# Performance work log

Hardware: AMD Instinct MI355X
Metric: run time of the kernel (lower is better)

Reference implementation:

```python
import jax, jax.numpy as jnp
import numpy as np

B, T, DM, DS = 8, 2048, 1024, 256
BASE_DECAY = 0.05


def _lin(k, out_dim, in_dim):
    return jax.random.normal(k, (out_dim, in_dim), jnp.float32) / np.sqrt(in_dim).astype(np.float32)


def setup_inputs() -> dict:
    key = jax.random.key(0)
    ks = jax.random.split(key, 18)
    return {
        "x": jax.random.normal(ks[0], (B, T, DM), jnp.float32),
        "prev_state": jax.random.normal(ks[1], (B, DS), jnp.float32),
        "W_in": _lin(ks[2], DS, DM),
        "W_x": _lin(ks[3], DS, DM),
        "W_s": _lin(ks[4], DS, DS),
        "W_out": _lin(ks[5], DM, DS),
        "W_gx": _lin(ks[6], DS, DM),
        "b_gx": jax.random.normal(ks[7], (DS,), jnp.float32) * 0.02,
        "W_gs": _lin(ks[8], DS, DS),
        "b_gs": jax.random.normal(ks[9], (DS,), jnp.float32) * 0.02,
        "W_dc": _lin(ks[10], DS, DM + DS),
        "b_dc": jax.random.normal(ks[11], (DS,), jnp.float32) * 0.02,
        "W_pp": _lin(ks[12], DS, 2 * DS),
        "b_pp": jax.random.normal(ks[13], (DS,), jnp.float32) * 0.02,
        "W_pg": _lin(ks[14], DS, DS),
        "b_pg": jax.random.normal(ks[15], (DS,), jnp.float32) * 0.02,
    }


def reference(x, prev_state, W_in, W_x, W_s, W_out, W_gx, b_gx, W_gs, b_gs,
              W_dc, b_dc, W_pp, b_pp, W_pg, b_pg):
    # torch Linear: y = x @ W.T (+ b); W is [out, in]
    lin = lambda v, W: jnp.einsum('bti,oi->bto', v, W)
    Bx, Tx, _ = x.shape
    delta = lin(x, W_in)                                   # [B,T,DS]
    s_prev = jnp.broadcast_to(prev_state[:, None, :], (Bx, Tx, prev_state.shape[-1]))
    ctx = jnp.concatenate([x, s_prev], axis=-1)            # [B,T,DM+DS]
    decay = jnp.exp(-BASE_DECAY * jnp.clip(jax.nn.sigmoid(lin(ctx, W_dc) + b_dc), 0.0, 1.0))
    s_pred = s_prev * decay + delta + lin(x, W_x) + 0.5 * lin(s_prev, W_s)
    perturb_in = jnp.concatenate([s_pred, s_prev], axis=-1)  # [B,T,2*DS]
    perturb_vec = jnp.tanh(lin(perturb_in, W_pp) + b_pp)
    perturb_strength = jax.nn.sigmoid(lin(s_prev, W_pg) + b_pg)
    s_corrected = s_pred + perturb_strength * perturb_vec
    gate_in = jax.nn.sigmoid(lin(x, W_gx) + b_gx)
    gate_state = jax.nn.sigmoid(lin(s_prev, W_gs) + b_gs)
    h = s_corrected * gate_in * gate_state
    out = lin(h, W_out)                                    # [B,T,DM]
    return out, h[:, -1, :]
```

## Files before the change

kernel.cpp:

```cpp
#include <hip/hip_runtime.h>
#include <hip/hip_bf16.h>
#include <math.h>


typedef __attribute__((ext_vector_type(4)))  float f32x4;
typedef __attribute__((ext_vector_type(8)))  short bf16x8;

#define DEV static __device__ __forceinline__

DEV float bf2f(short u) {
  union { float f; unsigned i; } v; v.i = ((unsigned)(unsigned short)u) << 16; return v.f;
}
DEV short f2bf(float f) {
  union { float f; unsigned i; } v; v.f = f;
  unsigned x = v.i;
  return (short)((x + 0x7fffu + ((x >> 16) & 1u)) >> 16);
}
DEV unsigned pk_bf16(float lo, float hi) {
  __hip_bfloat162 h = __float22bfloat162_rn(make_float2(lo, hi));
  return *(unsigned*)&h;
}
DEV float sigmoidf_(float x) { return 1.f / (1.f + expf(-x)); }

DEV void gl16(const void* g, void* l) {
  __builtin_amdgcn_global_load_lds(
      (const __attribute__((address_space(1))) void*)(g),
      (__attribute__((address_space(3))) void*)(l), 16, 0, 0);
}

DEV void stage_tile(const short* gA, const short* gB, short* As, short* Bs,
                    int lda, int ldb, int w, int lane) {
  const int rsub = lane >> 2, kc = (lane & 3) * 8;
#pragma unroll
  for (int j = 0; j < 2; ++j) {
    const int seg = w * 2 + j;
    const int r = seg * 16 + rsub;
    gl16(gA + (size_t)r * lda + kc, As + seg * 512);
    gl16(gB + (size_t)r * ldb + kc, Bs + seg * 512);
  }
}

DEV void kstep(const short* Asb, const short* Bsb, int wr, int wc, int arow, int ag,
               f32x4 (&acc)[4][4]) {
  bf16x8 af[4], bfv[4];
#pragma unroll
  for (int mi = 0; mi < 4; ++mi)
    af[mi] = *(const bf16x8*)(Asb + (wr * 64 + mi * 16 + arow) * 32 + ag * 8);
#pragma unroll
  for (int ni = 0; ni < 4; ++ni)
    bfv[ni] = *(const bf16x8*)(Bsb + (wc * 64 + ni * 16 + arow) * 32 + ag * 8);
#pragma unroll
  for (int mi = 0; mi < 4; ++mi)
#pragma unroll
    for (int ni = 0; ni < 4; ++ni)
      acc[mi][ni] = __builtin_amdgcn_mfma_f32_16x16x32_bf16(af[mi], bfv[ni], acc[mi][ni], 0, 0, 0);
}

static const size_t OFF_S    = 0;
static const size_t OFF_G    = 8388608;
static const size_t OFF_XBF  = 25165824;
static const size_t OFF_WCAT = OFF_XBF + 33554432;
static const size_t OFF_WPP  = OFF_WCAT + 1572864;
static const size_t OFF_WOUT = OFF_WPP + 131072;
static const size_t OFF_VEC  = OFF_WOUT + 524288;

__global__ __launch_bounds__(256, 1) void prep_all_k(
    const float* __restrict__ x, short* __restrict__ xbf,
    const float* __restrict__ W_in, const float* __restrict__ W_x,
    const float* __restrict__ W_gx, const float* __restrict__ W_dc,
    const float* __restrict__ W_pp, const float* __restrict__ W_out,
    short* __restrict__ wcat, short* __restrict__ wpp, short* __restrict__ wout,
    const float* __restrict__ prev, const float* __restrict__ Ws,
    const float* __restrict__ bdc, const float* __restrict__ bpp,
    const float* __restrict__ Wpg, const float* __restrict__ bpg,
    const float* __restrict__ Wgs, const float* __restrict__ bgs,
    float* __restrict__ vecs) {
  const int bid = (int)blockIdx.x, tid = (int)threadIdx.x;
  if (bid < 8192) {
    const size_t i = ((size_t)bid * 256 + tid) * 8;
    const float4 a = *(const float4*)(x + i);
    const float4 b = *(const float4*)(x + i + 4);
    uint4 o;
    o.x = pk_bf16(a.x, a.y); o.y = pk_bf16(a.z, a.w);
    o.z = pk_bf16(b.x, b.y); o.w = pk_bf16(b.z, b.w);
    *(uint4*)(xbf + i) = o;
  } else if (bid < 12544) {
    const int idx = (bid - 8192) * 256 + tid;
    const int N_WCAT = 768 * 1024, N_WPP = 256 * 256;
    if (idx < N_WCAT) {
      const int r = idx >> 10, k = idx & 1023;
      const int g = r / 96, j = r % 96;
      float v;
      if (j < 32)      v = W_in[(g * 32 + j) * 1024 + k] + W_x[(g * 32 + j) * 1024 + k];
      else if (j < 64) v = W_gx[(g * 32 + j - 32) * 1024 + k];
      else             v = W_dc[(g * 32 + j - 64) * 1280 + k];
      wcat[idx] = f2bf(v);
    } else if (idx < N_WCAT + N_WPP) {
      const int j = idx - N_WCAT, o = j >> 8, k = j & 255;
      wpp[j] = f2bf(W_pp[o * 512 + k]);
    } else {
      const int j = idx - N_WCAT - N_WPP, o = j >> 8, k = j & 255;
      wout[j] = f2bf(W_out[o * 256 + k]);
    }
  } else {
    const int sb = bid - 12544;
    const int b = sb / 20, rem = sb % 20, m = rem >> 2, oq = rem & 3;
    const int lane = tid & 63, w = tid >> 6;
    const float4 sv = *(const float4*)(prev + b * 256 + lane * 4);
    const float* Wb; const float* bias; int stride, off;
    if (m == 0)      { Wb = W_dc; stride = 1280; off = 1024; bias = bdc; }
    else if (m == 1) { Wb = Ws;   stride = 256;  off = 0;    bias = nullptr; }
    else if (m == 2) { Wb = W_pp; stride = 512;  off = 256;  bias = bpp; }
    else if (m == 3) { Wb = Wpg;  stride = 256;  off = 0;    bias = bpg; }
    else             { Wb = Wgs;  stride = 256;  off = 0;    bias = bgs; }
    const int o0 = oq * 64 + w * 16;
#pragma unroll 4
    for (int i = 0; i < 16; ++i) {
      const int o = o0 + i;
      const float4 wv = *(const float4*)(Wb + (size_t)o * stride + off + lane * 4);
      float p = wv.x * sv.x + wv.y * sv.y + wv.z * sv.z + wv.w * sv.w;
#pragma unroll
      for (int d = 32; d >= 1; d >>= 1) p += __shfl_xor(p, d, 64);
      if (lane == 0) {
        float r = (m == 1) ? 0.5f * p : p + bias[o];
        if (m >= 3) r = sigmoidf_(r);
        vecs[m * 2048 + b * 256 + o] = r;
      }
    }
  }
}

__global__ __launch_bounds__(256) void gemm1sg_k(const short* __restrict__ A,
                                                 const short* __restrict__ Bm,
                                                 const float* __restrict__ prev,
                                                 const float* __restrict__ bgx,
                                                 const float* __restrict__ vecs,
                                                 short* __restrict__ S,
                                                 short* __restrict__ G) {
  __shared__ short As[2][4096];
  __shared__ short Bs[2][3072];
  const int tid = (int)threadIdx.x, lane = tid & 63, w = tid >> 6;
  int bid = (int)blockIdx.x;
  bid = (bid & 7) * 128 + (bid >> 3);
  const int mt = bid >> 3, ntg = bid & 7;
  const int m0 = mt * 128, b = m0 >> 11;
  const short* gA = A + (size_t)m0 * 1024;
  const short* gB = Bm + (size_t)(ntg * 96) * 1024;
  const int rsub = lane >> 2, kc = (lane & 3) * 8;

  f32x4 acc[2][6];
#pragma unroll
  for (int mi = 0; mi < 2; ++mi)
#pragma unroll
    for (int ni = 0; ni < 6; ++ni)
#pragma unroll
      for (int r = 0; r < 4; ++r) acc[mi][ni][r] = 0.f;

#define STAGE1(buf, t)                                                        \
  {                                                                           \
    _Pragma("unroll")                                                         \
    for (int j = 0; j < 2; ++j) {                                             \
      const int seg = w * 2 + j;                                              \
      gl16(gA + (size_t)(seg * 16 + rsub) * 1024 + (t) * 32 + kc,             \
           As[buf] + seg * 512);                                              \
    }                                                                         \
    {                                                                         \
      const int Gr = w * 64 + lane;                                           \
      gl16(gB + (size_t)(Gr >> 2) * 1024 + (t) * 32 + ((Gr & 3) * 8),         \
           Bs[buf] + w * 512);                                                \
    }                                                                         \
    if (w < 2) {                                                              \
      const int Gr = 256 + w * 64 + lane;                                     \
      gl16(gB + (size_t)(Gr >> 2) * 1024 + (t) * 32 + ((Gr & 3) * 8),         \
           Bs[buf] + 2048 + w * 512);                                         \
    }                                                                         \
  }

  STAGE1(0, 0);
  __syncthreads();
  const int arow = lane & 15, ag = lane >> 4;
#pragma unroll 1
  for (int t = 0; t < 32; ++t) {
    if (t < 31) STAGE1((t + 1) & 1, t + 1);
    const short* Asb = As[t & 1];
    const short* Bsb = Bs[t & 1];
    bf16x8 af[2];
#pragma unroll
    for (int mi = 0; mi < 2; ++mi)
      af[mi] = *(const bf16x8*)(Asb + (w * 32 + mi * 16 + arow) * 32 + ag * 8);
#pragma unroll
    for (int ni = 0; ni < 6; ++ni) {
      const bf16x8 bf = *(const bf16x8*)(Bsb + (ni * 16 + arow) * 32 + ag * 8);
#pragma unroll
      for (int mi = 0; mi < 2; ++mi)
        acc[mi][ni] = __builtin_amdgcn_mfma_f32_16x16x32_bf16(af[mi], bf, acc[mi][ni], 0, 0, 0);
    }
    __syncthreads();
  }
#undef STAGE1

  const int quad = lane >> 4;
#pragma unroll
  for (int nj = 0; nj < 2; ++nj) {
    const int cg = ntg * 32 + nj * 16 + arow;
    const float sdc = vecs[0 * 2048 + b * 256 + cg];
    const float sws = vecs[1 * 2048 + b * 256 + cg];
    const float pv  = prev[b * 256 + cg];
    const float bg  = bgx[cg];
#pragma unroll
    for (int mi = 0; mi < 2; ++mi)
#pragma unroll
      for (int r = 0; r < 4; ++r) {
        const int row = m0 + w * 32 + mi * 16 + quad * 4 + r;
        const float dec = expf(-0.05f * sigmoidf_(acc[mi][4 + nj][r] + sdc));
        const float sp = pv * dec + acc[mi][nj][r] + sws;
        const float g = sigmoidf_(acc[mi][2 + nj][r] + bg);
        S[(size_t)row * 256 + cg] = f2bf(sp);
        G[(size_t)row * 256 + cg] = f2bf(g);
      }
  }
}

__global__ __launch_bounds__(256) void gemm2h_k(const short* __restrict__ S,
                                                const short* __restrict__ G,
                                                const short* __restrict__ Wpp,
                                                const float* __restrict__ vecs,
                                                short* __restrict__ H,
                                                float* __restrict__ out) {
  __shared__ short As[2][4096];
  __shared__ short Bs[2][4096];
  const int tid = (int)threadIdx.x, lane = tid & 63, w = tid >> 6;
  const int wr = w >> 1, wc = w & 1;
  int bid = (int)blockIdx.x;
  bid = (bid & 7) * 32 + (bid >> 3);
  const int m0 = (bid >> 1) * 128, n0 = (bid & 1) * 128;
  const int b = m0 >> 11;
  const short* gA = S + (size_t)m0 * 256;
  const short* gB = Wpp + (size_t)n0 * 256;

  f32x4 acc[4][4];
#pragma unroll
  for (int mi = 0; mi < 4; ++mi)
#pragma unroll
    for (int ni = 0; ni < 4; ++ni)
#pragma unroll
      for (int r = 0; r < 4; ++r) acc[mi][ni][r] = 0.f;

  stage_tile(gA, gB, As[0], Bs[0], 256, 256, w, lane);
  __syncthreads();
  const int arow = lane & 15, ag = lane >> 4;
#pragma unroll 1
  for (int t = 0; t < 8; ++t) {
    if (t < 7)
      stage_tile(gA + (t + 1) * 32, gB + (t + 1) * 32,
                 As[(t + 1) & 1], Bs[(t + 1) & 1], 256, 256, w, lane);
    kstep(As[t & 1], Bs[t & 1], wr, wc, arow, ag, acc);
    __syncthreads();
  }
#pragma unroll
  for (int mi = 0; mi < 4; ++mi)
#pragma unroll
    for (int ni = 0; ni < 4; ++ni) {
      const int col = n0 + wc * 64 + ni * 16 + (lane & 15);
      const float spp  = vecs[2 * 2048 + b * 256 + col];
      const float pstr = vecs[3 * 2048 + b * 256 + col];
      const float gst  = vecs[4 * 2048 + b * 256 + col];
#pragma unroll
      for (int r = 0; r < 4; ++r) {
        const int row = m0 + wr * 64 + mi * 16 + (lane >> 4) * 4 + r;
        const float pv = tanhf(acc[mi][ni][r] + spp);
        const float sp = bf2f(S[(size_t)row * 256 + col]);
        const float h = (sp + pstr * pv) * bf2f(G[(size_t)row * 256 + col]) * gst;
        H[(size_t)row * 256 + col] = f2bf(h);
        if ((row & 2047) == 2047) out[16777216 + b * 256 + col] = h;
      }
    }
}

__global__ __launch_bounds__(256) void gemm3_k(const short* __restrict__ H,
                                               const short* __restrict__ Wout,
                                               float* __restrict__ out) {
  __shared__ short As[2][4096];
  __shared__ short Bs[2][4096];
  const int tid = (int)threadIdx.x, lane = tid & 63, w = tid >> 6;
  const int wr = w >> 1, wc = w & 1;
  int bid = (int)blockIdx.x;
  bid = (bid & 7) * 128 + (bid >> 3);
  const int m0 = (bid >> 3) * 128, n0 = (bid & 7) * 128;
  const short* gA = H + (size_t)m0 * 256;
  const short* gB = Wout + (size_t)n0 * 256;

  f32x4 acc[4][4];
#pragma unroll
  for (int mi = 0; mi < 4; ++mi)
#pragma unroll
    for (int ni = 0; ni < 4; ++ni)
#pragma unroll
      for (int r = 0; r < 4; ++r) acc[mi][ni][r] = 0.f;

  stage_tile(gA, gB, As[0], Bs[0], 256, 256, w, lane);
  __syncthreads();
  const int arow = lane & 15, ag = lane >> 4;
#pragma unroll 1
  for (int t = 0; t < 8; ++t) {
    if (t < 7)
      stage_tile(gA + (t + 1) * 32, gB + (t + 1) * 32,
                 As[(t + 1) & 1], Bs[(t + 1) & 1], 256, 256, w, lane);
    kstep(As[t & 1], Bs[t & 1], wr, wc, arow, ag, acc);
    __syncthreads();
  }
#pragma unroll
  for (int mi = 0; mi < 4; ++mi)
#pragma unroll
    for (int ni = 0; ni < 4; ++ni) {
      const int col = n0 + wc * 64 + ni * 16 + (lane & 15);
#pragma unroll
      for (int r = 0; r < 4; ++r) {
        const int row = m0 + wr * 64 + mi * 16 + (lane >> 4) * 4 + r;
        out[(size_t)row * 1024 + col] = acc[mi][ni][r];
      }
    }
}

extern "C" void kernel_launch(void* const* d_in, const int* in_sizes, int n_in,
                              void* d_out, int out_size, void* d_ws, size_t ws_size,
                              hipStream_t stream) {
  (void)in_sizes; (void)n_in; (void)out_size; (void)ws_size;
  const float* x      = (const float*)d_in[0];
  const float* prev   = (const float*)d_in[1];
  const float* W_in   = (const float*)d_in[2];
  const float* W_x    = (const float*)d_in[3];
  const float* W_s    = (const float*)d_in[4];
  const float* W_out  = (const float*)d_in[5];
  const float* W_gx   = (const float*)d_in[6];
  const float* b_gx   = (const float*)d_in[7];
  const float* W_gs   = (const float*)d_in[8];
  const float* b_gs   = (const float*)d_in[9];
  const float* W_dc   = (const float*)d_in[10];
  const float* b_dc   = (const float*)d_in[11];
  const float* W_pp   = (const float*)d_in[12];
  const float* b_pp   = (const float*)d_in[13];
  const float* W_pg   = (const float*)d_in[14];
  const float* b_pg   = (const float*)d_in[15];

  char* ws = (char*)d_ws;
  short* S    = (short*)(ws + OFF_S);
  short* G    = (short*)(ws + OFF_G);
  short* xbf  = (short*)(ws + OFF_XBF);
  short* H    = (short*)(ws + OFF_XBF);
  short* wcat = (short*)(ws + OFF_WCAT);
  short* wpp  = (short*)(ws + OFF_WPP);
  short* wout = (short*)(ws + OFF_WOUT);
  float* vecs = (float*)(ws + OFF_VEC);
  float* out  = (float*)d_out;

  prep_all_k<<<12704, 256, 0, stream>>>(x, xbf, W_in, W_x, W_gx, W_dc, W_pp, W_out,
                                        wcat, wpp, wout, prev, W_s, b_dc, b_pp,
                                        W_pg, b_pg, W_gs, b_gs, vecs);
  gemm1sg_k<<<1024, 256, 0, stream>>>(xbf, wcat, prev, b_gx, vecs, S, G);
  gemm2h_k<<<256, 256, 0, stream>>>(S, G, wpp, vecs, H, out);
  gemm3_k<<<1024, 256, 0, stream>>>(H, wout, out);
}
```

Baseline: 109.5 us.

## Triple-buffer gemm1sg LDS tiles with explicit vmcnt waits and raw barriers

Replaces the double-buffered K-loop in the first fused GEMM with a three-stage LDS ring. Global-to-LDS loads are issued two tiles ahead, and the loop waits on a partial s_waitcnt vmcnt instead of a full __syncthreads, so more memory latency can overlap with MFMA work. To keep the load mapping uniform, the B tile now loads 128 rows per stage while only 96 are used. That adds wasted traffic and LDS, and may read past the weight rows for the last column group.

Result: slower. 119.5 us (+9.1%).

```diff
diff --git a/kernel.cpp b/kernel.cpp
--- a/kernel.cpp
+++ b/kernel.cpp
@@ -137,8 +137,8 @@
                                                  const float* __restrict__ vecs,
                                                  short* __restrict__ S,
                                                  short* __restrict__ G) {
-  __shared__ short As[2][4096];
-  __shared__ short Bs[2][3072];
+  __shared__ short As[3][4096];
+  __shared__ short Bs[3][4096];
   const int tid = (int)threadIdx.x, lane = tid & 63, w = tid >> 6;
   int bid = (int)blockIdx.x;
   bid = (bid & 7) * 128 + (bid >> 3);
@@ -156,34 +156,36 @@
 #pragma unroll
       for (int r = 0; r < 4; ++r) acc[mi][ni][r] = 0.f;
 
-#define STAGE1(buf, t)                                                        \
+#define STAGE(s, t)                                                           \
   {                                                                           \
     _Pragma("unroll")                                                         \
     for (int j = 0; j < 2; ++j) {                                             \
       const int seg = w * 2 + j;                                              \
-      gl16(gA + (size_t)(seg * 16 + rsub) * 1024 + (t) * 32 + kc,             \
-           As[buf] + seg * 512);                                              \
+      const size_t roff = (size_t)(seg * 16 + rsub) * 1024 + (size_t)(t) * 32 + kc; \
+      gl16(gA + roff, As[s] + seg * 512);                                     \
+      gl16(gB + roff, Bs[s] + seg * 512);                                     \
     }                                                                         \
-    {                                                                         \
-      const int Gr = w * 64 + lane;                                           \
-      gl16(gB + (size_t)(Gr >> 2) * 1024 + (t) * 32 + ((Gr & 3) * 8),         \
-           Bs[buf] + w * 512);                                                \
-    }                                                                         \
-    if (w < 2) {                                                              \
-      const int Gr = 256 + w * 64 + lane;                                     \
-      gl16(gB + (size_t)(Gr >> 2) * 1024 + (t) * 32 + ((Gr & 3) * 8),         \
-           Bs[buf] + 2048 + w * 512);                                         \
-    }                                                                         \
-  }
-
-  STAGE1(0, 0);
-  __syncthreads();
+  }
+
+  STAGE(0, 0);
+  STAGE(1, 1);
   const int arow = lane & 15, ag = lane >> 4;
+  int cur = 0;
 #pragma unroll 1
   for (int t = 0; t < 32; ++t) {
-    if (t < 31) STAGE1((t + 1) & 1, t + 1);
-    const short* Asb = As[t & 1];
-    const short* Bsb = Bs[t & 1];
+    int pre = cur + 2; if (pre >= 3) pre -= 3;
+    if (t < 30) {
+      STAGE(pre, t + 2);
+      asm volatile("s_waitcnt vmcnt(8)" ::: "memory");
+    } else if (t == 30) {
+      asm volatile("s_waitcnt vmcnt(4)" ::: "memory");
+    } else {
+      asm volatile("s_waitcnt vmcnt(0)" ::: "memory");
+    }
+    __builtin_amdgcn_s_barrier();
+    __builtin_amdgcn_sched_barrier(0);
+    const short* Asb = As[cur];
+    const short* Bsb = Bs[cur];
     bf16x8 af[2];
 #pragma unroll
     for (int mi = 0; mi < 2; ++mi)
@@ -195,9 +197,10 @@
       for (int mi = 0; mi < 2; ++mi)
         acc[mi][ni] = __builtin_amdgcn_mfma_f32_16x16x32_bf16(af[mi], bf, acc[mi][ni], 0, 0, 0);
     }
-    __syncthreads();
-  }
-#undef STAGE1
+    __builtin_amdgcn_s_barrier();
+    cur = (cur == 2) ? 0 : cur + 1;
+  }
+#undef STAGE
 
   const int quad = lane >> 4;
 #pragma unroll
```
